# Performance work log

Hardware: AMD Instinct MI355X
Metric: run time of the kernel (lower is better)

The kernel has to match this reference:

```python
import jax, jax.numpy as jnp
import numpy as np

MIN_LOOP = 4  # min_hairpin
INF = jnp.float32(1e18)


def _nussinov_ptr(e_pair, e_unp, allowed, min_loop=MIN_LOOP):
    """Fill the O(L^2) DP table span-by-span (anti-diagonal wavefront),
    vectorized over the start index i within each span. Returns the
    backpointer table ptr (L,L) int32 with the same encoding as the
    original numpy code: 0=i unpaired, 1=j unpaired, 2=(i,j) pair, k+3=bifurcation at k."""
    L = e_unp.shape[0]
    d = jnp.arange(L)
    dp = jnp.full((L, L), INF, dtype=jnp.float32).at[d, d].set(e_unp)
    ptr = jnp.full((L, L), -1, dtype=jnp.int32).at[d, d].set(0)
    ii = jnp.arange(L)
    tt = jnp.arange(L)  # bifurcation offset t = k - i, valid for t <= s-2

    def span_body(s, carry):
        dp, ptr = carry
        jj = ii + s - 1                      # true j; >= L entries are dropped on scatter
        jc = jnp.minimum(jj, L - 1)          # clamped j for safe gathers
        ic1 = jnp.minimum(ii + 1, L - 1)
        # candidate 0: i unpaired -> dp[i+1, j] + e_unp[i]
        c0 = dp[ic1, jc] + e_unp[ii]
        # candidate 1: j unpaired -> dp[i, j-1] + e_unp[j]
        c1 = dp[ii, jnp.maximum(jc - 1, 0)] + e_unp[jc]
        # candidate 2: (i,j) paired -> dp[i+1, j-1] + e_pair[i,j] (inner=0 when span==2)
        inner = jnp.where(s >= 3, dp[ic1, jnp.maximum(jc - 1, 0)], jnp.float32(0.0))
        c2 = inner + e_pair[ii, jc]
        pair_ok = allowed[ii, jc] & (jc - ii > min_loop)
        # bifurcation: min over k=i+t, t in [0, s-2]: dp[i,k] + dp[k+1,j]
        kk = ii[:, None] + tt[None, :]
        kc = jnp.minimum(kk, L - 1)
        bif = jnp.where(tt[None, :] <= s - 2,
                        dp[ii[:, None], kc] + dp[jnp.minimum(kc + 1, L - 1), jc[:, None]],
                        INF)
        t_arg = jnp.argmin(bif, axis=1)  # first occurrence == ascending-k tie-break
        bif_min = jnp.take_along_axis(bif, t_arg[:, None], axis=1)[:, 0]
        # sequential strict-< selection, matching the numpy candidate order
        best = c0
        bp = jnp.zeros(L, jnp.int32)
        u = c1 < best; best = jnp.where(u, c1, best); bp = jnp.where(u, 1, bp)
        u = pair_ok & (c2 < best); best = jnp.where(u, c2, best); bp = jnp.where(u, 2, bp)
        u = bif_min < best; best = jnp.where(u, bif_min, best)
        bp = jnp.where(u, (ii + t_arg + 3).astype(jnp.int32), bp)
        dp = dp.at[ii, jj].set(best, mode='drop')
        ptr = ptr.at[ii, jj].set(bp, mode='drop')
        return dp, ptr

    dp, ptr = jax.lax.fori_loop(2, L + 1, span_body, (dp, ptr))
    return ptr


def _backtrace(ptr):
    """Iterative stack-based backtrace (LIFO, same push order as numpy).
    Intervals on the stack are disjoint, so depth <= L; size 2L for slack."""
    L = ptr.shape[0]
    S = 2 * L
    stack0 = jnp.zeros((S, 2), jnp.int32).at[0].set(jnp.array([0, L - 1], jnp.int32))
    res0 = jnp.full((L,), -1, jnp.int32)

    def cond(st):
        return st[1] > 0

    def body(st):
        stack, sp, res = st
        sp1 = sp - 1
        i = stack[sp1, 0]
        j = stack[sp1, 1]
        p = ptr[i, j]
        valid = i < j
        is0 = p == 0; is1 = p == 1; is2 = p == 2
        k = p - 3
        # first push (popped slot is reused)
        e1i = jnp.where(is0, i + 1, jnp.where(is1, i, jnp.where(is2, i + 1, i)))
        e1j = jnp.where(is0, j, jnp.where(is1, j - 1, jnp.where(is2, j - 1, k)))
        v1 = valid & jnp.where(is2, (i + 1) <= (j - 1), True)
        # second push only for bifurcation: (k+1, j)
        v2 = valid & (p >= 3)
        do_pair = valid & is2
        res = res.at[i].set(jnp.where(do_pair, j, res[i]))
        res = res.at[j].set(jnp.where(do_pair, i, res[j]))
        stack = stack.at[sp1].set(jnp.where(v1, jnp.stack([e1i, e1j]), stack[sp1]))
        sp_a = sp1 + v1.astype(jnp.int32)
        slot = jnp.minimum(sp_a, S - 1)
        stack = stack.at[slot].set(jnp.where(v2, jnp.stack([k + 1, j]), stack[slot]))
        sp_b = sp_a + v2.astype(jnp.int32)
        return stack, sp_b, res

    _, _, res = jax.lax.while_loop(cond, body, (stack0, jnp.int32(1), res0))
    return res


def _decode(e_pair, e_unp, pair_mask):
    ptr = jax.vmap(_nussinov_ptr, in_axes=(0, 0, 0))(e_pair, e_unp, pair_mask)
    return jax.vmap(_backtrace)(ptr)  # (B, L) int32, -1 = unpaired


def setup_inputs() -> dict:
    key = jax.random.key(0)
    k1, k2, k3 = jax.random.split(key, 3)
    B, L = 16, 512
    e_pair = jax.random.normal(k1, (B, L, L), dtype=jnp.float32)
    e_unp = jax.random.normal(k2, (B, L), dtype=jnp.float32)
    pair_mask = jax.random.bernoulli(k3, 0.3, (B, L, L))
    return {"e_pair": e_pair, "e_unp": e_unp, "pair_mask": pair_mask}


def reference(e_pair, e_unp, pair_mask):
    return _decode(e_pair, e_unp, pair_mask)
```

## Files before the change

kernel.cpp:

```cpp
#include <hip/hip_runtime.h>
#include <stdint.h>

#define L_ 512
#define NBUF (L_ * L_)
#define T_ 64
#define NT_ 8
#define INFV 3.0e38f

__global__ __launch_bounds__(1024) void fd_mask_probe(const unsigned int* __restrict__ pm,
                                                      int n32,
                                                      unsigned int* __restrict__ flags) {
    __shared__ unsigned int sf;
    if (threadIdx.x == 0) sf = 0u;
    __syncthreads();
    unsigned int local = 0;
    const int nscan = n32 < 65536 ? n32 : 65536;
    for (int idx = threadIdx.x; idx < nscan; idx += 1024) {
        const unsigned int w = pm[idx];
        const unsigned int h0 = w & 0xFFFFu, h1 = w >> 16;
        if (w > 1u) local |= 1u;
        if (w & 0xFEFEFEFEu) local |= 2u;
        if ((h0 != 0u && h0 != 0x3F80u) || (h1 != 0u && h1 != 0x3F80u)) local |= 4u;
        if (w == 0x3F803F80u || w == 0x00003F80u) local |= 8u;
        if ((h0 != 0u && h0 != 0x3C00u) || (h1 != 0u && h1 != 0x3C00u)) local |= 16u;
    }
    if (local) atomicOr(&sf, local);
    __syncthreads();
    if (threadIdx.x == 0) flags[0] = sf;
}

__device__ __forceinline__ int mask_mode(unsigned int f) {
    if (!(f & 1u)) return 0;
    if (!(f & 2u)) return 1;
    if (!(f & 4u)) return (f & 8u) ? 3 : 2;
    return (!(f & 16u)) ? 3 : 2;
}

__device__ __forceinline__ bool mask_bit(int mode, const unsigned int* pmW,
                                         const unsigned char* pm8,
                                         const unsigned short* pm16,
                                         const float* pmf, size_t gi) {
    if (mode == 0) return pmW[gi] != 0u;
    if (mode == 1) return pm8[gi] != 0;
    if (mode == 3) return pm16[gi] != 0;
    return pmf[gi] != 0.0f;
}

__global__ __launch_bounds__(256) void fd_diag(
    const float* __restrict__ e_pair, const float* __restrict__ e_unp,
    const unsigned int* __restrict__ pm, const unsigned int* __restrict__ flags,
    float* __restrict__ dp_ws, unsigned short* __restrict__ ptr_ws)
{
    const int b = blockIdx.x / NT_;
    const int I = blockIdx.x % NT_;
    const int t = threadIdx.x;
    const int r0 = I * T_;
    const float* ep = e_pair + (size_t)b * NBUF;
    float* dp = dp_ws + (size_t)b * NBUF;
    unsigned short* ptr = ptr_ws + (size_t)b * NBUF;
    const int mode = mask_mode(flags[0]);
    const unsigned int*   pmW  = pm + (size_t)b * NBUF;
    const unsigned char*  pm8  = ((const unsigned char*) pm) + (size_t)b * NBUF;
    const unsigned short* pm16 = ((const unsigned short*)pm) + (size_t)b * NBUF;
    const float*          pmf  = ((const float*)         pm) + (size_t)b * NBUF;

    __shared__ float Ct[T_][T_ + 4];
    __shared__ float epl[T_][T_ + 4];
    __shared__ unsigned char mkb[T_][T_ + 4];
    __shared__ unsigned short bp[T_][T_ + 4];
    __shared__ float eu[T_];

    for (int e = t; e < T_ * T_; e += 256) {
        const int r = e >> 6, c = e & 63;
        const size_t gi = (size_t)(r0 + r) * L_ + r0 + c;
        epl[r][c] = ep[gi];
        mkb[r][c] = mask_bit(mode, pmW, pm8, pm16, pmf, gi) ? 1 : 0;
    }
    if (t < T_) eu[t] = e_unp[(size_t)b * L_ + r0 + t];
    __syncthreads();
    if (t < T_) Ct[t][t] = eu[t];
    __syncthreads();

    const int cell = t >> 2, sub = t & 3;
    for (int m = 1; m < T_; ++m) {
        if (cell < T_ - m) {
            const int ti = cell, tj = cell + m;
            float mv = INFV; int km = 0;
            for (int tk = ti + sub; tk < tj; tk += 4) {
                const float v = Ct[ti][tk] + Ct[tk + 1][tj];
                if (v < mv) { mv = v; km = tk; }
            }
            for (int off = 1; off < 4; off <<= 1) {
                const float ov = __shfl_xor(mv, off, 4);
                const int   ok = __shfl_xor(km, off, 4);
                if (ov < mv || (ov == mv && ok < km)) { mv = ov; km = ok; }
            }
            if (sub == 0) {
                const float c0 = Ct[ti + 1][tj] + eu[ti];
                const float c1 = Ct[ti][tj - 1] + eu[tj];
                const float inner = (m >= 2) ? Ct[ti + 1][tj - 1] : 0.0f;
                const float c2 = inner + epl[ti][tj];
                const bool pok = mkb[ti][tj] && (m > 4);
                float best = c0; int bv = 0;
                if (c1 < best)        { best = c1; bv = 1; }
                if (pok && c2 < best) { best = c2; bv = 2; }
                if (mv < best)        { best = mv; bv = r0 + km + 3; }
                Ct[ti][tj] = best;
                bp[ti][tj] = (unsigned short)bv;
            }
        }
        __syncthreads();
    }
    for (int e = t; e < T_ * T_; e += 256) {
        const int r = e >> 6, c = e & 63;
        if (c >= r) {
            const size_t gi = (size_t)(r0 + r) * L_ + r0 + c;
            dp[gi] = Ct[r][c];
            if (c > r) ptr[gi] = bp[r][c];
        }
    }
}

__global__ __launch_bounds__(256) void fd_step(
    const float* __restrict__ e_pair, const float* __restrict__ e_unp,
    const unsigned int* __restrict__ pm, const unsigned int* __restrict__ flags,
    float* __restrict__ dp_ws, unsigned short* __restrict__ ptr_ws,
    int* __restrict__ out, int d, int nI, int do_bt)
{
    const int b = blockIdx.x / nI;
    const int I = blockIdx.x % nI;
    const int J = I + d;
    const int t = threadIdx.x;
    const int r0 = I * T_, q0 = J * T_;
    const float* ep = e_pair + (size_t)b * NBUF;
    float* dp = dp_ws + (size_t)b * NBUF;
    unsigned short* ptr = ptr_ws + (size_t)b * NBUF;
    const int mode = mask_mode(flags[0]);
    const unsigned int*   pmW  = pm + (size_t)b * NBUF;
    const unsigned char*  pm8  = ((const unsigned char*) pm) + (size_t)b * NBUF;
    const unsigned short* pm16 = ((const unsigned short*)pm) + (size_t)b * NBUF;
    const float*          pmf  = ((const float*)         pm) + (size_t)b * NBUF;

    __shared__ float SA[T_][T_ + 4];
    __shared__ float SB[T_][T_ + 4];
    __shared__ float Ct[T_][T_ + 4];
    __shared__ float accv[T_][T_ + 4];
    __shared__ unsigned short acck[T_][T_ + 4];
    __shared__ float epl[T_][T_ + 4];
    __shared__ unsigned char mkb[T_][T_ + 4];
    __shared__ unsigned short bp[T_][T_ + 4];
    __shared__ float euI[T_], euJ[T_], rowB[T_], colL[T_];
    __shared__ float cornerS;
    __shared__ int sti[2 * L_], stj[2 * L_];

    float av[16]; int akr[16];
    const int ti0 = (t >> 4) * 4, tj0 = (t & 15) * 4;
#pragma unroll
    for (int q = 0; q < 16; ++q) { av[q] = INFV; akr[q] = 0; }
    for (int K = I + 1; K < J; ++K) {
        const int kb = K * T_;
        __syncthreads();
        for (int e = t; e < T_ * T_; e += 256) {
            const int r = e >> 6, c = e & 63;
            SA[r][c] = dp[(size_t)(r0 + r) * L_ + kb + c];
            SB[r][c] = dp[(size_t)(kb + 1 + r) * L_ + q0 + c];
        }
        __syncthreads();
        for (int kk = 0; kk < T_; ++kk) {
            float a[4], bb[4];
#pragma unroll
            for (int r = 0; r < 4; ++r) a[r] = SA[ti0 + r][kk];
#pragma unroll
            for (int c = 0; c < 4; ++c) bb[c] = SB[kk][tj0 + c];
            const int kg = kb + kk;
#pragma unroll
            for (int r = 0; r < 4; ++r)
#pragma unroll
                for (int c = 0; c < 4; ++c) {
                    const float v = a[r] + bb[c];
                    const int q = r * 4 + c;
                    if (v < av[q]) { av[q] = v; akr[q] = kg; }
                }
        }
    }
    __syncthreads();
#pragma unroll
    for (int r = 0; r < 4; ++r)
#pragma unroll
        for (int c = 0; c < 4; ++c) {
            accv[ti0 + r][tj0 + c] = av[r * 4 + c];
            acck[ti0 + r][tj0 + c] = (unsigned short)akr[r * 4 + c];
        }

    for (int e = t; e < T_ * T_; e += 256) {
        const int r = e >> 6, c = e & 63;
        SA[r][c] = dp[(size_t)(r0 + r) * L_ + r0 + c];
        SB[r][c] = dp[(size_t)(q0 + r) * L_ + q0 + c];
        const size_t gi = (size_t)(r0 + r) * L_ + q0 + c;
        epl[r][c] = ep[gi];
        mkb[r][c] = mask_bit(mode, pmW, pm8, pm16, pmf, gi) ? 1 : 0;
    }
    if (t < T_) {
        euI[t] = e_unp[(size_t)b * L_ + r0 + t];
        euJ[t] = e_unp[(size_t)b * L_ + q0 + t];
        rowB[t] = dp[(size_t)(r0 + T_) * L_ + q0 + t];
        colL[t] = dp[(size_t)(r0 + t) * L_ + q0 - 1];
    }
    if (t == 0) cornerS = (d >= 2) ? dp[(size_t)(r0 + T_) * L_ + q0 - 1] : 0.0f;
    __syncthreads();

    const int cell = t >> 2, sub = t & 3;
    for (int m = -(T_ - 1); m <= T_ - 1; ++m) {
        const int am = m < 0 ? -m : m;
        if (cell < T_ - am) {
            const int ti = (m < 0) ? cell - m : cell;
            const int tj = ti + m;
            const int span = d * T_ + m;
            float mv = INFV; int km = 0;
            for (int tk = ti + sub; tk < T_; tk += 4) {
                const float dk1j = (tk < T_ - 1) ? Ct[tk + 1][tj] : rowB[tj];
                const float v = SA[ti][tk] + dk1j;
                if (v < mv) { mv = v; km = r0 + tk; }
            }
            for (int tk = sub; tk < tj; tk += 4) {
                const float v = Ct[ti][tk] + SB[tk + 1][tj];
                if (v < mv) { mv = v; km = q0 + tk; }
            }
            for (int off = 1; off < 4; off <<= 1) {
                const float ov = __shfl_xor(mv, off, 4);
                const int   ok = __shfl_xor(km, off, 4);
                if (ov < mv || (ov == mv && ok < km)) { mv = ov; km = ok; }
            }
            if (sub == 0) {
                const float bvv = accv[ti][tj]; const int bvk = acck[ti][tj];
                if (bvv < mv || (bvv == mv && bvk < km)) { mv = bvv; km = bvk; }
                const float c0 = ((ti < T_ - 1) ? Ct[ti + 1][tj] : rowB[tj]) + euI[ti];
                const float c1 = ((tj > 0) ? Ct[ti][tj - 1] : colL[ti]) + euJ[tj];
                float inner;
                if (span == 1)          inner = 0.0f;
                else if (ti < T_ - 1)   inner = (tj > 0) ? Ct[ti + 1][tj - 1] : colL[ti + 1];
                else                    inner = (tj > 0) ? rowB[tj - 1] : cornerS;
                const float c2 = inner + epl[ti][tj];
                const bool pok = mkb[ti][tj] && (span > 4);
                float best = c0; int bv = 0;
                if (c1 < best)        { best = c1; bv = 1; }
                if (pok && c2 < best) { best = c2; bv = 2; }
                if (mv < best)        { best = mv; bv = km + 3; }
                Ct[ti][tj] = best;
                bp[ti][tj] = (unsigned short)bv;
            }
        }
        __syncthreads();
    }

    for (int e = t; e < T_ * T_; e += 256) {
        const int r = e >> 6, c = e & 63;
        const size_t gi = (size_t)(r0 + r) * L_ + q0 + c;
        dp[gi] = Ct[r][c];
        ptr[gi] = bp[r][c];
    }

    if (do_bt) {
        int* res = out + (size_t)b * L_;
        for (int idx = t; idx < L_; idx += 256) res[idx] = -1;
        __syncthreads();
        if (t == 0) {
            int sp = 1; sti[0] = 0; stj[0] = L_ - 1;
            while (sp > 0) {
                --sp;
                const int i = sti[sp], j = stj[sp];
                if (i < j) {
                    int p;
                    if (i >= r0 && i < r0 + T_ && j >= q0 && j < q0 + T_)
                        p = bp[i - r0][j - q0];
                    else
                        p = ptr[(size_t)i * L_ + j];
                    if (p == 0)      { sti[sp] = i + 1; stj[sp] = j;     ++sp; }
                    else if (p == 1) { sti[sp] = i;     stj[sp] = j - 1; ++sp; }
                    else if (p == 2) {
                        res[i] = j; res[j] = i;
                        if (i + 1 <= j - 1) { sti[sp] = i + 1; stj[sp] = j - 1; ++sp; }
                    } else {
                        const int k = p - 3;
                        sti[sp] = i;     stj[sp] = k; ++sp;
                        sti[sp] = k + 1; stj[sp] = j; ++sp;
                    }
                }
            }
        }
    }
}

extern "C" void kernel_launch(void* const* d_in, const int* in_sizes, int n_in,
                              void* d_out, int out_size, void* d_ws, size_t ws_size,
                              hipStream_t stream) {
    const float* e_pair = (const float*)d_in[0];
    const float* e_unp  = (const float*)d_in[1];
    const unsigned int* pm = (const unsigned int*)d_in[2];
    const int B = in_sizes[1] / L_;
    int* out = (int*)d_out;

    unsigned int* flags = (unsigned int*)d_ws;
    float* dp_ws = (float*)((char*)d_ws + 256);
    unsigned short* ptr_ws = (unsigned short*)(dp_ws + (size_t)B * NBUF);

    const int n32 = in_sizes[2] / 4;
    fd_mask_probe<<<dim3(1), dim3(1024), 0, stream>>>(pm, n32, flags);
    fd_diag<<<dim3(B * NT_), dim3(256), 0, stream>>>(e_pair, e_unp, pm, flags,
                                                     dp_ws, ptr_ws);
    for (int d = 1; d < NT_; ++d) {
        const int nI = NT_ - d;
        fd_step<<<dim3(B * nI), dim3(256), 0, stream>>>(e_pair, e_unp, pm, flags,
                                                        dp_ws, ptr_ws, out,
                                                        d, nI, d == NT_ - 1 ? 1 : 0);
    }
}
```

Baseline: 2.254 ms.

## Use one thread per cell in tile wavefront, transpose tiles, split out backtrace kernel

The intra-tile anti-diagonal fill now gives each cell a single thread. That thread uses four independent min accumulators and reads row-contiguous data from a transposed copy of the tile and of the diagonal block, which replaces the four-lane shuffle reduction. Global loads and stores use float4 vectors, and the off-diagonal accumulation is skipped when d<2. The serial backtrace moves into its own kernel, which first streams the whole ptr table to warm the cache. The price is more shared memory (an extra transposed tile), lower lane use on short diagonals, and an extra launch.

```diff
diff --git a/kernel.cpp b/kernel.cpp
--- a/kernel.cpp
+++ b/kernel.cpp
@@ -125,7 +125,7 @@
     const float* __restrict__ e_pair, const float* __restrict__ e_unp,
     const unsigned int* __restrict__ pm, const unsigned int* __restrict__ flags,
     float* __restrict__ dp_ws, unsigned short* __restrict__ ptr_ws,
-    int* __restrict__ out, int d, int nI, int do_bt)
+    int d, int nI)
 {
     const int b = blockIdx.x / nI;
     const int I = blockIdx.x % nI;
@@ -142,8 +142,9 @@
     const float*          pmf  = ((const float*)         pm) + (size_t)b * NBUF;
 
     __shared__ float SA[T_][T_ + 4];
-    __shared__ float SB[T_][T_ + 4];
+    __shared__ float SBX[T_][T_ + 4];
     __shared__ float Ct[T_][T_ + 4];
+    __shared__ float CtT[T_][T_ + 4];
     __shared__ float accv[T_][T_ + 4];
     __shared__ unsigned short acck[T_][T_ + 4];
     __shared__ float epl[T_][T_ + 4];
@@ -151,54 +152,59 @@
     __shared__ unsigned short bp[T_][T_ + 4];
     __shared__ float euI[T_], euJ[T_], rowB[T_], colL[T_];
     __shared__ float cornerS;
-    __shared__ int sti[2 * L_], stj[2 * L_];
-
-    float av[16]; int akr[16];
-    const int ti0 = (t >> 4) * 4, tj0 = (t & 15) * 4;
-#pragma unroll
-    for (int q = 0; q < 16; ++q) { av[q] = INFV; akr[q] = 0; }
-    for (int K = I + 1; K < J; ++K) {
-        const int kb = K * T_;
-        __syncthreads();
-        for (int e = t; e < T_ * T_; e += 256) {
-            const int r = e >> 6, c = e & 63;
-            SA[r][c] = dp[(size_t)(r0 + r) * L_ + kb + c];
-            SB[r][c] = dp[(size_t)(kb + 1 + r) * L_ + q0 + c];
-        }
-        __syncthreads();
-        for (int kk = 0; kk < T_; ++kk) {
-            float a[4], bb[4];
-#pragma unroll
-            for (int r = 0; r < 4; ++r) a[r] = SA[ti0 + r][kk];
-#pragma unroll
-            for (int c = 0; c < 4; ++c) bb[c] = SB[kk][tj0 + c];
-            const int kg = kb + kk;
-#pragma unroll
-            for (int r = 0; r < 4; ++r)
-#pragma unroll
-                for (int c = 0; c < 4; ++c) {
-                    const float v = a[r] + bb[c];
-                    const int q = r * 4 + c;
-                    if (v < av[q]) { av[q] = v; akr[q] = kg; }
-                }
-        }
-    }
-    __syncthreads();
-#pragma unroll
-    for (int r = 0; r < 4; ++r)
-#pragma unroll
-        for (int c = 0; c < 4; ++c) {
-            accv[ti0 + r][tj0 + c] = av[r * 4 + c];
-            acck[ti0 + r][tj0 + c] = (unsigned short)akr[r * 4 + c];
-        }
-
+
+    if (d >= 2) {
+        float av[16]; int akr[16];
+        const int ti0 = (t >> 4) * 4, tj0 = (t & 15) * 4;
+#pragma unroll
+        for (int q = 0; q < 16; ++q) { av[q] = INFV; akr[q] = 0; }
+        for (int K = I + 1; K < J; ++K) {
+            const int kb = K * T_;
+            __syncthreads();
+            for (int e = t; e < T_ * T_ / 4; e += 256) {
+                const int r = e >> 4, c4 = (e & 15) * 4;
+                *(float4*)&SA[r][c4]  = *(const float4*)&dp[(size_t)(r0 + r) * L_ + kb + c4];
+                *(float4*)&SBX[r][c4] = *(const float4*)&dp[(size_t)(kb + 1 + r) * L_ + q0 + c4];
+            }
+            __syncthreads();
+            for (int kk = 0; kk < T_; ++kk) {
+                float a[4], bb[4];
+#pragma unroll
+                for (int r = 0; r < 4; ++r) a[r] = SA[ti0 + r][kk];
+#pragma unroll
+                for (int c = 0; c < 4; ++c) bb[c] = SBX[kk][tj0 + c];
+                const int kg = kb + kk;
+#pragma unroll
+                for (int r = 0; r < 4; ++r)
+#pragma unroll
+                    for (int c = 0; c < 4; ++c) {
+                        const float v = a[r] + bb[c];
+                        const int q = r * 4 + c;
+                        if (v < av[q]) { av[q] = v; akr[q] = kg; }
+                    }
+            }
+        }
+#pragma unroll
+        for (int r = 0; r < 4; ++r)
+#pragma unroll
+            for (int c = 0; c < 4; ++c) {
+                accv[ti0 + r][tj0 + c] = av[r * 4 + c];
+                acck[ti0 + r][tj0 + c] = (unsigned short)akr[r * 4 + c];
+            }
+    }
+    __syncthreads();
+
+    for (int e = t; e < T_ * T_ / 4; e += 256) {
+        const int r = e >> 4, c4 = (e & 15) * 4;
+        *(float4*)&SA[r][c4]  = *(const float4*)&dp[(size_t)(r0 + r) * L_ + r0 + c4];
+        const float4 vj = *(const float4*)&dp[(size_t)(q0 + r) * L_ + q0 + c4];
+        SBX[c4 + 0][r] = vj.x; SBX[c4 + 1][r] = vj.y;
+        SBX[c4 + 2][r] = vj.z; SBX[c4 + 3][r] = vj.w;
+        *(float4*)&epl[r][c4] = *(const float4*)&ep[(size_t)(r0 + r) * L_ + q0 + c4];
+    }
     for (int e = t; e < T_ * T_; e += 256) {
         const int r = e >> 6, c = e & 63;
-        SA[r][c] = dp[(size_t)(r0 + r) * L_ + r0 + c];
-        SB[r][c] = dp[(size_t)(q0 + r) * L_ + q0 + c];
-        const size_t gi = (size_t)(r0 + r) * L_ + q0 + c;
-        epl[r][c] = ep[gi];
-        mkb[r][c] = mask_bit(mode, pmW, pm8, pm16, pmf, gi) ? 1 : 0;
+        mkb[r][c] = mask_bit(mode, pmW, pm8, pm16, pmf, (size_t)(r0 + r) * L_ + q0 + c) ? 1 : 0;
     }
     if (t < T_) {
         euI[t] = e_unp[(size_t)b * L_ + r0 + t];
@@ -209,82 +215,119 @@
     if (t == 0) cornerS = (d >= 2) ? dp[(size_t)(r0 + T_) * L_ + q0 - 1] : 0.0f;
     __syncthreads();
 
-    const int cell = t >> 2, sub = t & 3;
     for (int m = -(T_ - 1); m <= T_ - 1; ++m) {
         const int am = m < 0 ? -m : m;
-        if (cell < T_ - am) {
-            const int ti = (m < 0) ? cell - m : cell;
+        const int ncell = T_ - am;
+        if (t < ncell) {
+            const int ti = (m < 0) ? t + am : t;
             const int tj = ti + m;
             const int span = d * T_ + m;
-            float mv = INFV; int km = 0;
-            for (int tk = ti + sub; tk < T_; tk += 4) {
-                const float dk1j = (tk < T_ - 1) ? Ct[tk + 1][tj] : rowB[tj];
-                const float v = SA[ti][tk] + dk1j;
-                if (v < mv) { mv = v; km = r0 + tk; }
-            }
-            for (int tk = sub; tk < tj; tk += 4) {
-                const float v = Ct[ti][tk] + SB[tk + 1][tj];
-                if (v < mv) { mv = v; km = q0 + tk; }
-            }
-            for (int off = 1; off < 4; off <<= 1) {
-                const float ov = __shfl_xor(mv, off, 4);
-                const int   ok = __shfl_xor(km, off, 4);
-                if (ov < mv || (ov == mv && ok < km)) { mv = ov; km = ok; }
-            }
-            if (sub == 0) {
-                const float bvv = accv[ti][tj]; const int bvk = acck[ti][tj];
-                if (bvv < mv || (bvv == mv && bvk < km)) { mv = bvv; km = bvk; }
-                const float c0 = ((ti < T_ - 1) ? Ct[ti + 1][tj] : rowB[tj]) + euI[ti];
-                const float c1 = ((tj > 0) ? Ct[ti][tj - 1] : colL[ti]) + euJ[tj];
-                float inner;
-                if (span == 1)          inner = 0.0f;
-                else if (ti < T_ - 1)   inner = (tj > 0) ? Ct[ti + 1][tj - 1] : colL[ti + 1];
-                else                    inner = (tj > 0) ? rowB[tj - 1] : cornerS;
-                const float c2 = inner + epl[ti][tj];
-                const bool pok = mkb[ti][tj] && (span > 4);
-                float best = c0; int bv = 0;
-                if (c1 < best)        { best = c1; bv = 1; }
-                if (pok && c2 < best) { best = c2; bv = 2; }
-                if (mv < best)        { best = mv; bv = km + 3; }
-                Ct[ti][tj] = best;
-                bp[ti][tj] = (unsigned short)bv;
-            }
+            float v0 = INFV, v1 = INFV, v2 = INFV, v3 = INFV;
+            int   k0 = 0,    k1 = 0,    k2 = 0,    k3 = 0;
+            int tk = ti;
+            for (; tk + 4 <= T_ - 1; tk += 4) {
+                const float x0 = SA[ti][tk + 0] + CtT[tj][tk + 1];
+                const float x1 = SA[ti][tk + 1] + CtT[tj][tk + 2];
+                const float x2 = SA[ti][tk + 2] + CtT[tj][tk + 3];
+                const float x3 = SA[ti][tk + 3] + CtT[tj][tk + 4];
+                if (x0 < v0) { v0 = x0; k0 = r0 + tk + 0; }
+                if (x1 < v1) { v1 = x1; k1 = r0 + tk + 1; }
+                if (x2 < v2) { v2 = x2; k2 = r0 + tk + 2; }
+                if (x3 < v3) { v3 = x3; k3 = r0 + tk + 3; }
+            }
+            for (; tk < T_ - 1; ++tk) {
+                const float x = SA[ti][tk] + CtT[tj][tk + 1];
+                if (x < v0) { v0 = x; k0 = r0 + tk; }
+            }
+            { const float x = SA[ti][T_ - 1] + rowB[tj];
+              if (x < v1) { v1 = x; k1 = r0 + T_ - 1; } }
+            tk = 0;
+            for (; tk + 4 <= tj; tk += 4) {
+                const float x0 = Ct[ti][tk + 0] + SBX[tj][tk + 1];
+                const float x1 = Ct[ti][tk + 1] + SBX[tj][tk + 2];
+                const float x2 = Ct[ti][tk + 2] + SBX[tj][tk + 3];
+                const float x3 = Ct[ti][tk + 3] + SBX[tj][tk + 4];
+                if (x0 < v0) { v0 = x0; k0 = q0 + tk + 0; }
+                if (x1 < v1) { v1 = x1; k1 = q0 + tk + 1; }
+                if (x2 < v2) { v2 = x2; k2 = q0 + tk + 2; }
+                if (x3 < v3) { v3 = x3; k3 = q0 + tk + 3; }
+            }
+            for (; tk < tj; ++tk) {
+                const float x = Ct[ti][tk] + SBX[tj][tk + 1];
+                if (x < v2) { v2 = x; k2 = q0 + tk; }
+            }
+            float mv = v0; int km = k0;
+            if (v1 < mv || (v1 == mv && k1 < km)) { mv = v1; km = k1; }
+            if (v2 < mv || (v2 == mv && k2 < km)) { mv = v2; km = k2; }
+            if (v3 < mv || (v3 == mv && k3 < km)) { mv = v3; km = k3; }
+            if (d >= 2) {
+                const float bv = accv[ti][tj]; const int bk = acck[ti][tj];
+                if (bv < mv || (bv == mv && bk < km)) { mv = bv; km = bk; }
+            }
+            const float c0 = ((ti < T_ - 1) ? Ct[ti + 1][tj] : rowB[tj]) + euI[ti];
+            const float c1 = ((tj > 0) ? Ct[ti][tj - 1] : colL[ti]) + euJ[tj];
+            float inner;
+            if (span == 1)        inner = 0.0f;
+            else if (ti < T_ - 1) inner = (tj > 0) ? Ct[ti + 1][tj - 1] : colL[ti + 1];
+            else                  inner = (tj > 0) ? rowB[tj - 1] : cornerS;
+            const float c2 = inner + epl[ti][tj];
+            const bool pok = mkb[ti][tj] && (span > 4);
+            float best = c0; int bv2 = 0;
+            if (c1 < best)        { best = c1; bv2 = 1; }
+            if (pok && c2 < best) { best = c2; bv2 = 2; }
+            if (mv < best)        { best = mv; bv2 = km + 3; }
+            Ct[ti][tj] = best;
+            CtT[tj][ti] = best;
+            bp[ti][tj] = (unsigned short)bv2;
         }
         __syncthreads();
     }
 
+    for (int e = t; e < T_ * T_ / 4; e += 256) {
+        const int r = e >> 4, c4 = (e & 15) * 4;
+        *(float4*)&dp[(size_t)(r0 + r) * L_ + q0 + c4] = *(const float4*)&Ct[r][c4];
+    }
     for (int e = t; e < T_ * T_; e += 256) {
         const int r = e >> 6, c = e & 63;
-        const size_t gi = (size_t)(r0 + r) * L_ + q0 + c;
-        dp[gi] = Ct[r][c];
-        ptr[gi] = bp[r][c];
-    }
-
-    if (do_bt) {
-        int* res = out + (size_t)b * L_;
-        for (int idx = t; idx < L_; idx += 256) res[idx] = -1;
-        __syncthreads();
-        if (t == 0) {
-            int sp = 1; sti[0] = 0; stj[0] = L_ - 1;
-            while (sp > 0) {
-                --sp;
-                const int i = sti[sp], j = stj[sp];
-                if (i < j) {
-                    int p;
-                    if (i >= r0 && i < r0 + T_ && j >= q0 && j < q0 + T_)
-                        p = bp[i - r0][j - q0];
-                    else
-                        p = ptr[(size_t)i * L_ + j];
-                    if (p == 0)      { sti[sp] = i + 1; stj[sp] = j;     ++sp; }
-                    else if (p == 1) { sti[sp] = i;     stj[sp] = j - 1; ++sp; }
-                    else if (p == 2) {
-                        res[i] = j; res[j] = i;
-                        if (i + 1 <= j - 1) { sti[sp] = i + 1; stj[sp] = j - 1; ++sp; }
-                    } else {
-                        const int k = p - 3;
-                        sti[sp] = i;     stj[sp] = k; ++sp;
-                        sti[sp] = k + 1; stj[sp] = j; ++sp;
-                    }
+        ptr[(size_t)(r0 + r) * L_ + q0 + c] = bp[r][c];
+    }
+}
+
+__global__ __launch_bounds__(256) void fd_backtrace(
+    const unsigned short* __restrict__ ptr_ws, int* __restrict__ out)
+{
+    const int b = blockIdx.x;
+    const int t = threadIdx.x;
+    const unsigned short* ptr = ptr_ws + (size_t)b * NBUF;
+    int* res = out + (size_t)b * L_;
+    __shared__ int sti[2 * L_], stj[2 * L_];
+
+    const uint4* p4 = (const uint4*)ptr;
+    unsigned int acc = 0;
+    for (int idx = t; idx < NBUF / 8; idx += 256) {
+        const uint4 v = p4[idx];
+        acc += v.x ^ v.y ^ v.z ^ v.w;
+    }
+    asm volatile("" :: "v"(acc));
+    for (int idx = t; idx < L_; idx += 256) res[idx] = -1;
+    __syncthreads();
+
+    if (t == 0) {
+        int sp = 1; sti[0] = 0; stj[0] = L_ - 1;
+        while (sp > 0) {
+            --sp;
+            const int i = sti[sp], j = stj[sp];
+            if (i < j) {
+                const int p = (int)ptr[(size_t)i * L_ + j];
+                if (p == 0)      { sti[sp] = i + 1; stj[sp] = j;     ++sp; }
+                else if (p == 1) { sti[sp] = i;     stj[sp] = j - 1; ++sp; }
+                else if (p == 2) {
+                    res[i] = j; res[j] = i;
+                    if (i + 1 <= j - 1) { sti[sp] = i + 1; stj[sp] = j - 1; ++sp; }
+                } else {
+                    const int k = p - 3;
+                    sti[sp] = i;     stj[sp] = k; ++sp;
+                    sti[sp] = k + 1; stj[sp] = j; ++sp;
                 }
             }
         }
@@ -311,7 +354,7 @@
     for (int d = 1; d < NT_; ++d) {
         const int nI = NT_ - d;
         fd_step<<<dim3(B * nI), dim3(256), 0, stream>>>(e_pair, e_unp, pm, flags,
-                                                        dp_ws, ptr_ws, out,
-                                                        d, nI, d == NT_ - 1 ? 1 : 0);
-    }
-}
+                                                        dp_ws, ptr_ws, d, nI);
+    }
+    fd_backtrace<<<dim3(B), dim3(256), 0, stream>>>(ptr_ws, out);
+}
```

Result: slower. 3.066 ms (+36.0%).
